# Optimization experiments

Hardware: AMD Instinct MI355X
Metric: run time of the kernel (lower is better)

## Reference

```python
import jax, jax.numpy as jnp
import numpy as np

N_ENTITY = 64368
N_REL = 40
DIM = 128
N_BASES = 8
N_EDGES = 500000
BATCH = 64
SEED_LEN = 32


def _glorot(k, shape, gain=1.414):
    fan_in, fan_out = shape[0], shape[1]
    bound = gain * np.sqrt(6.0 / (fan_in + fan_out))
    return jax.random.uniform(k, shape, jnp.float32, -bound, bound)


def setup_inputs() -> dict:
    key = jax.random.key(0)
    ks = jax.random.split(key, 11)
    return dict(
        seed_ids=jax.random.randint(ks[0], (BATCH, SEED_LEN), 0, N_ENTITY),
        edge_src=jax.random.randint(ks[1], (N_EDGES,), 0, N_ENTITY),
        edge_dst=jax.random.randint(ks[2], (N_EDGES,), 0, N_ENTITY),
        edge_type=jax.random.randint(ks[3], (N_EDGES,), 0, N_REL),
        basis=jax.random.normal(ks[4], (N_BASES, N_ENTITY, DIM), jnp.float32) * 0.02,
        att=jax.random.normal(ks[5], (N_REL, N_BASES), jnp.float32) * 0.1,
        root=jax.random.normal(ks[6], (N_ENTITY, DIM), jnp.float32) * 0.02,
        rgcn_bias=jnp.zeros((DIM,), jnp.float32),
        attn_a=_glorot(ks[7], (DIM, DIM)),
        attn_b=_glorot(ks[8], (DIM, 1)),
        out_bias=jnp.zeros((N_ENTITY,), jnp.float32),
    )


def _rgcn_nodes(basis, att, root, rgcn_bias, edge_src, edge_dst, edge_type):
    # RGCNConv with x=None: message for edge e is row src[e] of w[type[e]],
    # where w = att @ basis (basis decomposition); 'mean' aggregation to dst;
    # update: aggr + root + bias.
    n_entity, dim = root.shape
    coeff = att[edge_type]  # [E, nb]
    agg = jnp.zeros((n_entity, dim), jnp.float32)
    for b in range(basis.shape[0]):  # small fixed loop over bases
        m = basis[b][edge_src] * coeff[:, b][:, None]  # [E, dim]
        agg = agg + jax.ops.segment_sum(m, edge_dst, num_segments=n_entity)
    deg = jax.ops.segment_sum(jnp.ones_like(edge_dst, jnp.float32), edge_dst,
                              num_segments=n_entity)
    agg = agg / jnp.maximum(deg, 1.0)[:, None]
    return agg + root + rgcn_bias[None, :]


def reference(seed_ids, edge_src, edge_dst, edge_type, basis, att, root,
              rgcn_bias, attn_a, attn_b, out_bias):
    nodes = _rgcn_nodes(basis, att, root, rgcn_bias, edge_src, edge_dst, edge_type)
    # self-attention pooling over each seed set (all entries valid / non-empty)
    H = nodes[seed_ids]  # [B, S, D]
    e = jnp.einsum('bsd,d->bs', jnp.tanh(jnp.einsum('bsd,de->bse', H, attn_a)),
                   attn_b[:, 0])  # [B, S]
    attn = jax.nn.softmax(e, axis=-1)
    u = jnp.einsum('bs,bsd->bd', attn, H)  # [B, D]
    # scores = F.linear(u, nodes_features, output.bias)
    scores = u @ nodes.T + out_bias[None, :]  # [B, n_entity]
    return scores
```

## Files before the change

kernel.cpp:

```cpp
#include <hip/hip_runtime.h>
#include <hip/hip_bf16.h>

#define N_ENTITY 64368
#define N_REL 40
#define DIM 128
#define N_BASES 8
#define N_EDGES 500000
#define BATCH 64
#define SEED_LEN 32
#define NROWS (BATCH * SEED_LEN)
#define SCAN_NB ((N_ENTITY + 255) / 256)
#define NPAD (SCAN_NB * 256)

__global__ __launch_bounds__(256) void k_hist2(
    const int* __restrict__ edst, const int* __restrict__ esrc,
    int* __restrict__ hist2)
{
    int e = blockIdx.x * 256 + threadIdx.x;
    if (e < N_EDGES) {
        atomicAdd(&hist2[edst[e]], 1);
        atomicAdd(&hist2[NPAD + esrc[e]], 1);
    }
}

__global__ __launch_bounds__(256) void k_scan1(
    const int* __restrict__ hist2, int* __restrict__ ptr2,
    int* __restrict__ partial)
{
    __shared__ int s[256];
    int tid = threadIdx.x;
    int gid = blockIdx.x * 256 + tid;
    int v = hist2[gid];
    s[tid] = v;
    __syncthreads();
    for (int off = 1; off < 256; off <<= 1) {
        int t = (tid >= off) ? s[tid - off] : 0;
        __syncthreads();
        s[tid] += t;
        __syncthreads();
    }
    ptr2[gid] = s[tid] - v;
    if (tid == 255) partial[blockIdx.x] = s[255];
}

__global__ __launch_bounds__(256) void k_scan2(
    const int* __restrict__ partial, int* __restrict__ poff)
{
    __shared__ int s[256];
    int tid = threadIdx.x;
    int base = blockIdx.x * SCAN_NB;
    int v = (tid < SCAN_NB) ? partial[base + tid] : 0;
    s[tid] = v;
    __syncthreads();
    for (int off = 1; off < 256; off <<= 1) {
        int t = (tid >= off) ? s[tid - off] : 0;
        __syncthreads();
        s[tid] += t;
        __syncthreads();
    }
    if (tid < SCAN_NB) poff[base + tid] = s[tid] - v;
}

__global__ __launch_bounds__(256) void k_scan3(
    int* __restrict__ ptr2, const int* __restrict__ poff,
    int* __restrict__ work2)
{
    int gid = blockIdx.x * 256 + threadIdx.x;
    int p = ptr2[gid] + poff[blockIdx.x];
    ptr2[gid] = p;
    work2[gid] = p;
}

__global__ __launch_bounds__(256) void k_scatter2(
    const int* __restrict__ esrc, const int* __restrict__ edst,
    const int* __restrict__ etype, int* __restrict__ work2,
    int* __restrict__ payload)
{
    int e = blockIdx.x * 256 + threadIdx.x;
    if (e < N_EDGES) {
        int dpos = atomicAdd(&work2[edst[e]], 1);
        int spos = atomicAdd(&work2[NPAD + esrc[e]], 1);
        payload[spos] = dpos * 64 + etype[e];
    }
}

__global__ __launch_bounds__(256) void k_scatterD(
    const int* __restrict__ esrc, const int* __restrict__ edst,
    const int* __restrict__ etype, int* __restrict__ work2,
    int* __restrict__ meta)
{
    int e = blockIdx.x * 256 + threadIdx.x;
    if (e < N_EDGES) {
        int pos = atomicAdd(&work2[edst[e]], 1);
        meta[pos] = esrc[e] * 64 + etype[e];
    }
}

__global__ __launch_bounds__(256) void k_phaseA(
    const int* __restrict__ sptr, const int* __restrict__ shist,
    const int* __restrict__ payload, const float* __restrict__ basis,
    const float* __restrict__ att, float* __restrict__ msg)
{
    __shared__ float att_s[N_REL * N_BASES];
    int tid = threadIdx.x;
    for (int i = tid; i < N_REL * N_BASES; i += 256) att_s[i] = att[i];
    __syncthreads();

    int sid = (blockIdx.x * 256 + tid) >> 5;
    int l32 = tid & 31;
    if (sid >= N_ENTITY) return;
    int cnt = shist[sid];
    if (cnt == 0) return;
    int p = sptr[sid];

    const size_t bstride = (size_t)N_ENTITY * DIM;
    const float* bp = basis + (size_t)sid * DIM + l32 * 4;
    float4 r0 = *(const float4*)(bp + 0 * bstride);
    float4 r1 = *(const float4*)(bp + 1 * bstride);
    float4 r2 = *(const float4*)(bp + 2 * bstride);
    float4 r3 = *(const float4*)(bp + 3 * bstride);
    float4 r4 = *(const float4*)(bp + 4 * bstride);
    float4 r5 = *(const float4*)(bp + 5 * bstride);
    float4 r6 = *(const float4*)(bp + 6 * bstride);
    float4 r7 = *(const float4*)(bp + 7 * bstride);

    int j = 0;
    for (; j + 1 < cnt; j += 2) {
        int plA = payload[p + j];
        int plB = payload[p + j + 1];
        const float* cA = att_s + (plA & 63) * N_BASES;
        const float* cB = att_s + (plB & 63) * N_BASES;
        float4 cA0 = *(const float4*)(cA);
        float4 cA1 = *(const float4*)(cA + 4);
        float4 cB0 = *(const float4*)(cB);
        float4 cB1 = *(const float4*)(cB + 4);

        float4 mA, mB;
        mA.x = cA0.x*r0.x + cA0.y*r1.x + cA0.z*r2.x + cA0.w*r3.x
             + cA1.x*r4.x + cA1.y*r5.x + cA1.z*r6.x + cA1.w*r7.x;
        mA.y = cA0.x*r0.y + cA0.y*r1.y + cA0.z*r2.y + cA0.w*r3.y
             + cA1.x*r4.y + cA1.y*r5.y + cA1.z*r6.y + cA1.w*r7.y;
        mA.z = cA0.x*r0.z + cA0.y*r1.z + cA0.z*r2.z + cA0.w*r3.z
             + cA1.x*r4.z + cA1.y*r5.z + cA1.z*r6.z + cA1.w*r7.z;
        mA.w = cA0.x*r0.w + cA0.y*r1.w + cA0.z*r2.w + cA0.w*r3.w
             + cA1.x*r4.w + cA1.y*r5.w + cA1.z*r6.w + cA1.w*r7.w;
        mB.x = cB0.x*r0.x + cB0.y*r1.x + cB0.z*r2.x + cB0.w*r3.x
             + cB1.x*r4.x + cB1.y*r5.x + cB1.z*r6.x + cB1.w*r7.x;
        mB.y = cB0.x*r0.y + cB0.y*r1.y + cB0.z*r2.y + cB0.w*r3.y
             + cB1.x*r4.y + cB1.y*r5.y + cB1.z*r6.y + cB1.w*r7.y;
        mB.z = cB0.x*r0.z + cB0.y*r1.z + cB0.z*r2.z + cB0.w*r3.z
             + cB1.x*r4.z + cB1.y*r5.z + cB1.z*r6.z + cB1.w*r7.z;
        mB.w = cB0.x*r0.w + cB0.y*r1.w + cB0.z*r2.w + cB0.w*r3.w
             + cB1.x*r4.w + cB1.y*r5.w + cB1.z*r6.w + cB1.w*r7.w;

        *(float4*)(msg + (size_t)(plA >> 6) * DIM + l32 * 4) = mA;
        *(float4*)(msg + (size_t)(plB >> 6) * DIM + l32 * 4) = mB;
    }
    if (j < cnt) {
        int plA = payload[p + j];
        const float* cA = att_s + (plA & 63) * N_BASES;
        float4 cA0 = *(const float4*)(cA);
        float4 cA1 = *(const float4*)(cA + 4);
        float4 mA;
        mA.x = cA0.x*r0.x + cA0.y*r1.x + cA0.z*r2.x + cA0.w*r3.x
             + cA1.x*r4.x + cA1.y*r5.x + cA1.z*r6.x + cA1.w*r7.x;
        mA.y = cA0.x*r0.y + cA0.y*r1.y + cA0.z*r2.y + cA0.w*r3.y
             + cA1.x*r4.y + cA1.y*r5.y + cA1.z*r6.y + cA1.w*r7.y;
        mA.z = cA0.x*r0.z + cA0.y*r1.z + cA0.z*r2.z + cA0.w*r3.z
             + cA1.x*r4.z + cA1.y*r5.z + cA1.z*r6.z + cA1.w*r7.z;
        mA.w = cA0.x*r0.w + cA0.y*r1.w + cA0.z*r2.w + cA0.w*r3.w
             + cA1.x*r4.w + cA1.y*r5.w + cA1.z*r6.w + cA1.w*r7.w;
        *(float4*)(msg + (size_t)(plA >> 6) * DIM + l32 * 4) = mA;
    }
}

__global__ __launch_bounds__(256) void k_phaseB(
    const int* __restrict__ dptr, const int* __restrict__ dhist,
    const float* __restrict__ msg, const float* __restrict__ root,
    const float* __restrict__ bias, float* __restrict__ agg)
{
    int wid  = (int)((blockIdx.x * 256 + threadIdx.x) >> 6);
    int lane = threadIdx.x & 63;
    if (wid >= N_ENTITY) return;
    int cnt = dhist[wid];
    int p   = dptr[wid];
    const float* mp = msg + (size_t)p * DIM + lane * 2;

    float ax = 0.f, ay = 0.f;
    int j = 0;
    for (; j + 3 < cnt; j += 4) {
        float2 v0 = *(const float2*)(mp + (size_t)(j + 0) * DIM);
        float2 v1 = *(const float2*)(mp + (size_t)(j + 1) * DIM);
        float2 v2 = *(const float2*)(mp + (size_t)(j + 2) * DIM);
        float2 v3 = *(const float2*)(mp + (size_t)(j + 3) * DIM);
        ax += (v0.x + v1.x) + (v2.x + v3.x);
        ay += (v0.y + v1.y) + (v2.y + v3.y);
    }
    for (; j < cnt; ++j) {
        float2 v = *(const float2*)(mp + (size_t)j * DIM);
        ax += v.x; ay += v.y;
    }

    float inv = 1.0f / fmaxf((float)cnt, 1.0f);
    int o = wid * DIM + lane * 2;
    float2 r  = *(const float2*)(root + o);
    float2 bb = *(const float2*)(bias + lane * 2);
    float2 outv;
    outv.x = ax * inv + r.x + bb.x;
    outv.y = ay * inv + r.y + bb.y;
    *(float2*)(agg + o) = outv;
}

#define ACC8(C0, C1, V0, V1, V2, V3, V4, V5, V6, V7)                         \
    acc.x += C0.x*V0.x + C0.y*V1.x + C0.z*V2.x + C0.w*V3.x                   \
           + C1.x*V4.x + C1.y*V5.x + C1.z*V6.x + C1.w*V7.x;                  \
    acc.y += C0.x*V0.y + C0.y*V1.y + C0.z*V2.y + C0.w*V3.y                   \
           + C1.x*V4.y + C1.y*V5.y + C1.z*V6.y + C1.w*V7.y;                  \
    acc.z += C0.x*V0.z + C0.y*V1.z + C0.z*V2.z + C0.w*V3.z                   \
           + C1.x*V4.z + C1.y*V5.z + C1.z*V6.z + C1.w*V7.z;                  \
    acc.w += C0.x*V0.w + C0.y*V1.w + C0.z*V2.w + C0.w*V3.w                   \
           + C1.x*V4.w + C1.y*V5.w + C1.z*V6.w + C1.w*V7.w;

__global__ __launch_bounds__(256) void k_gather(
    const int* __restrict__ ptr, const int* __restrict__ hist,
    const int* __restrict__ meta, const float* __restrict__ basis,
    const float* __restrict__ att, const float* __restrict__ root,
    const float* __restrict__ bias, float* __restrict__ agg)
{
    __shared__ float att_s[N_REL * N_BASES];
    int tid = threadIdx.x;
    for (int i = tid; i < N_REL * N_BASES; i += 256) att_s[i] = att[i];
    __syncthreads();

    int wid  = (int)((blockIdx.x * 256 + tid) >> 6);
    int lane = tid & 63;
    if (wid >= N_ENTITY) return;

    int half = lane >> 5;
    int l32  = lane & 31;
    int p   = ptr[wid];
    int cnt = hist[wid];
    const size_t bstride = (size_t)N_ENTITY * DIM;

    float4 acc = {0.f, 0.f, 0.f, 0.f};
    int j = 0;
    for (; j + 3 < cnt; j += 4) {
        int mA0 = meta[p + j + 0];
        int mA1 = meta[p + j + 1];
        int mB0 = meta[p + j + 2];
        int mB1 = meta[p + j + 3];
        int mA = half ? mA1 : mA0;
        int mB = half ? mB1 : mB0;
        const float* bA = basis + (size_t)(mA >> 6) * DIM + l32 * 4;
        const float* bB = basis + (size_t)(mB >> 6) * DIM + l32 * 4;
        float4 a0 = *(const float4*)(bA + 0 * bstride);
        float4 a1 = *(const float4*)(bA + 1 * bstride);
        float4 a2 = *(const float4*)(bA + 2 * bstride);
        float4 a3 = *(const float4*)(bA + 3 * bstride);
        float4 a4 = *(const float4*)(bA + 4 * bstride);
        float4 a5 = *(const float4*)(bA + 5 * bstride);
        float4 a6 = *(const float4*)(bA + 6 * bstride);
        float4 a7 = *(const float4*)(bA + 7 * bstride);
        float4 b0 = *(const float4*)(bB + 0 * bstride);
        float4 b1 = *(const float4*)(bB + 1 * bstride);
        float4 b2 = *(const float4*)(bB + 2 * bstride);
        float4 b3 = *(const float4*)(bB + 3 * bstride);
        float4 b4 = *(const float4*)(bB + 4 * bstride);
        float4 b5 = *(const float4*)(bB + 5 * bstride);
        float4 b6 = *(const float4*)(bB + 6 * bstride);
        float4 b7 = *(const float4*)(bB + 7 * bstride);
        float4 cA0 = *(const float4*)(att_s + (mA & 63) * N_BASES);
        float4 cA1 = *(const float4*)(att_s + (mA & 63) * N_BASES + 4);
        float4 cB0 = *(const float4*)(att_s + (mB & 63) * N_BASES);
        float4 cB1 = *(const float4*)(att_s + (mB & 63) * N_BASES + 4);
        ACC8(cA0, cA1, a0, a1, a2, a3, a4, a5, a6, a7)
        ACC8(cB0, cB1, b0, b1, b2, b3, b4, b5, b6, b7)
    }
    for (; j < cnt; j += 2) {
        int m0 = meta[p + j];
        bool has1 = (j + 1 < cnt);
        int m1 = has1 ? meta[p + j + 1] : m0;
        int m = half ? m1 : m0;
        float sc = (half && !has1) ? 0.0f : 1.0f;
        const float* bA = basis + (size_t)(m >> 6) * DIM + l32 * 4;
        float4 a0 = *(const float4*)(bA + 0 * bstride);
        float4 a1 = *(const float4*)(bA + 1 * bstride);
        float4 a2 = *(const float4*)(bA + 2 * bstride);
        float4 a3 = *(const float4*)(bA + 3 * bstride);
        float4 a4 = *(const float4*)(bA + 4 * bstride);
        float4 a5 = *(const float4*)(bA + 5 * bstride);
        float4 a6 = *(const float4*)(bA + 6 * bstride);
        float4 a7 = *(const float4*)(bA + 7 * bstride);
        float4 c0 = *(const float4*)(att_s + (m & 63) * N_BASES);
        float4 c1 = *(const float4*)(att_s + (m & 63) * N_BASES + 4);
        c0.x *= sc; c0.y *= sc; c0.z *= sc; c0.w *= sc;
        c1.x *= sc; c1.y *= sc; c1.z *= sc; c1.w *= sc;
        ACC8(c0, c1, a0, a1, a2, a3, a4, a5, a6, a7)
    }

    acc.x += __shfl_xor(acc.x, 32, 64);
    acc.y += __shfl_xor(acc.y, 32, 64);
    acc.z += __shfl_xor(acc.z, 32, 64);
    acc.w += __shfl_xor(acc.w, 32, 64);

    if (half == 0) {
        float inv = 1.0f / fmaxf((float)cnt, 1.0f);
        int o = wid * DIM + l32 * 4;
        float4 r  = *(const float4*)(root + o);
        float4 bb = *(const float4*)(bias + l32 * 4);
        float4 outv;
        outv.x = acc.x * inv + r.x + bb.x;
        outv.y = acc.y * inv + r.y + bb.y;
        outv.z = acc.z * inv + r.z + bb.z;
        outv.w = acc.w * inv + r.w + bb.w;
        *(float4*)(agg + o) = outv;
    }
}

__global__ __launch_bounds__(256) void k_attn_gemm(
    const int* __restrict__ seed_ids, const float* __restrict__ nodes,
    const float* __restrict__ A, float* __restrict__ T)
{
    __shared__ float As[DIM * 132];
    __shared__ float Hs[16 * DIM];

    int tid = threadIdx.x;
    int r0  = blockIdx.x * 16;

    for (int i = tid; i < DIM * DIM; i += 256) {
        int row = i >> 7, col = i & 127;
        As[row * 132 + col] = A[i];
    }
    for (int i = tid; i < 16 * DIM; i += 256) {
        int rr = i >> 7, d = i & 127;
        int nid = seed_ids[r0 + rr];
        Hs[rr * DIM + d] = nodes[(size_t)nid * DIM + d];
    }
    __syncthreads();

    int jx = tid & 31;
    int iy = tid >> 5;
    float acc[2][4] = {{0,0,0,0},{0,0,0,0}};

    for (int d = 0; d < DIM; ++d) {
        float h0 = Hs[(iy * 2 + 0) * DIM + d];
        float h1 = Hs[(iy * 2 + 1) * DIM + d];
        const float4 a4 = *(const float4*)(As + d * 132 + jx * 4);
        acc[0][0] += h0 * a4.x; acc[0][1] += h0 * a4.y;
        acc[0][2] += h0 * a4.z; acc[0][3] += h0 * a4.w;
        acc[1][0] += h1 * a4.x; acc[1][1] += h1 * a4.y;
        acc[1][2] += h1 * a4.z; acc[1][3] += h1 * a4.w;
    }
    #pragma unroll
    for (int i = 0; i < 2; ++i) {
        int r = r0 + iy * 2 + i;
        #pragma unroll
        for (int k = 0; k < 4; ++k)
            T[(size_t)r * DIM + jx * 4 + k] = tanhf(acc[i][k]);
    }
}

__global__ __launch_bounds__(256) void k_attn_pool(
    const int* __restrict__ seed_ids, const float* __restrict__ nodes,
    const float* __restrict__ T, const float* __restrict__ Bv,
    float* __restrict__ u, float* __restrict__ uT)
{
    __shared__ float part[SEED_LEN][9];
    __shared__ float attw[SEED_LEN];

    int b = blockIdx.x, tid = threadIdx.x;
    int s = tid >> 3, g = tid & 7;

    float pe = 0.0f;
    for (int jj = g; jj < DIM; jj += 8)
        pe += T[(size_t)(b * SEED_LEN + s) * DIM + jj] * Bv[jj];
    part[s][g] = pe;
    __syncthreads();

    if (tid < SEED_LEN) {
        float e = 0.0f;
        for (int k = 0; k < 8; ++k) e += part[tid][k];
        attw[tid] = e;
    }
    __syncthreads();

    if (tid == 0) {
        float mx = -1e30f;
        for (int k = 0; k < SEED_LEN; ++k) mx = fmaxf(mx, attw[k]);
        float ssum = 0.0f;
        for (int k = 0; k < SEED_LEN; ++k) {
            float v = expf(attw[k] - mx);
            attw[k] = v; ssum += v;
        }
        float inv = 1.0f / ssum;
        for (int k = 0; k < SEED_LEN; ++k) attw[k] *= inv;
    }
    __syncthreads();

    if (tid < DIM) {
        float acc = 0.0f;
        for (int k = 0; k < SEED_LEN; ++k) {
            int nid = seed_ids[b * SEED_LEN + k];
            acc += attw[k] * nodes[(size_t)nid * DIM + tid];
        }
        u[b * DIM + tid]  = acc;
        uT[tid * BATCH + b] = acc;
    }
}

__global__ __launch_bounds__(256) void k_scores(
    const float* __restrict__ nodes, const float* __restrict__ uT,
    const float* __restrict__ out_bias, float* __restrict__ out)
{
    __shared__ float Nl[DIM * 65];

    int tid = threadIdx.x;
    int n0  = blockIdx.x * 64;

    for (int i = tid; i < 64 * DIM; i += 256) {
        int n = i >> 7, d = i & 127;
        int gn = n0 + n;
        Nl[d * 65 + n] = (gn < N_ENTITY) ? nodes[(size_t)gn * DIM + d] : 0.0f;
    }
    __syncthreads();

    int w    = __builtin_amdgcn_readfirstlane(tid >> 6);
    int lane = tid & 63;
    int b0   = w * 16;

    float acc[16];
    #pragma unroll
    for (int k = 0; k < 16; ++k) acc[k] = 0.0f;

    #pragma unroll 4
    for (int d = 0; d < DIM; ++d) {
        float nv = Nl[d * 65 + lane];
        const float* up = uT + d * BATCH + b0;
        #pragma unroll
        for (int k = 0; k < 16; ++k) acc[k] += up[k] * nv;
    }

    int gn = n0 + lane;
    if (gn < N_ENTITY) {
        float ob = out_bias[gn];
        #pragma unroll
        for (int k = 0; k < 16; ++k)
            out[(size_t)(b0 + k) * N_ENTITY + gn] = acc[k] + ob;
    }
}

extern "C" void kernel_launch(void* const* d_in, const int* in_sizes, int n_in,
                              void* d_out, int out_size, void* d_ws, size_t ws_size,
                              hipStream_t stream)
{
    const int*   seed_ids  = (const int*)d_in[0];
    const int*   esrc      = (const int*)d_in[1];
    const int*   edst      = (const int*)d_in[2];
    const int*   etype     = (const int*)d_in[3];
    const float* basis     = (const float*)d_in[4];
    const float* att       = (const float*)d_in[5];
    const float* root      = (const float*)d_in[6];
    const float* rgcn_bias = (const float*)d_in[7];
    const float* attn_a    = (const float*)d_in[8];
    const float* attn_b    = (const float*)d_in[9];
    const float* out_bias  = (const float*)d_in[10];
    float* out = (float*)d_out;

    const size_t AGG_F  = (size_t)N_ENTITY * DIM;
    const size_t MSG_F  = (size_t)N_EDGES * DIM;
    const size_t H2_I   = (size_t)2 * NPAD;

    const size_t main_words = AGG_F + MSG_F + 3 * H2_I + 1024
                            + N_EDGES + (size_t)NROWS * DIM + 2 * BATCH * DIM;
    bool big = ws_size >= main_words * 4;

    if (big) {
        float* agg     = (float*)d_ws;
        float* msg     = agg + AGG_F;
        int*   hist2   = (int*)(msg + MSG_F);
        int*   ptr2    = hist2 + H2_I;
        int*   work2   = ptr2 + H2_I;
        int*   part2   = work2 + H2_I;
        int*   poff2   = part2 + 512;
        int*   payload = poff2 + 512;
        float* T       = (float*)(payload + N_EDGES);
        float* u       = T + (size_t)NROWS * DIM;
        float* uT      = u + BATCH * DIM;

        hipMemsetAsync(hist2, 0, H2_I * sizeof(int), stream);
        k_hist2<<<(N_EDGES + 255) / 256, 256, 0, stream>>>(edst, esrc, hist2);
        k_scan1<<<2 * SCAN_NB, 256, 0, stream>>>(hist2, ptr2, part2);
        k_scan2<<<2, 256, 0, stream>>>(part2, poff2);
        k_scan3<<<2 * SCAN_NB, 256, 0, stream>>>(ptr2, poff2, work2);
        k_scatter2<<<(N_EDGES + 255) / 256, 256, 0, stream>>>(
            esrc, edst, etype, work2, payload);

        k_phaseA<<<N_ENTITY / 8, 256, 0, stream>>>(
            ptr2 + NPAD, hist2 + NPAD, payload, basis, att, msg);
        k_phaseB<<<N_ENTITY / 4, 256, 0, stream>>>(
            ptr2, hist2, msg, root, rgcn_bias, agg);

        k_attn_gemm<<<NROWS / 16, 256, 0, stream>>>(seed_ids, agg, attn_a, T);
        k_attn_pool<<<BATCH, 256, 0, stream>>>(seed_ids, agg, T, attn_b, u, uT);
        k_scores<<<(N_ENTITY + 63) / 64, 256, 0, stream>>>(agg, uT, out_bias, out);
    } else {
        float* agg     = (float*)d_ws;
        int*   hist2   = (int*)(agg + AGG_F);
        int*   ptr2    = hist2 + H2_I;
        int*   work2   = ptr2 + H2_I;
        int*   part2   = work2 + H2_I;
        int*   poff2   = part2 + 512;
        int*   meta    = poff2 + 512;
        float* T       = (float*)(meta + N_EDGES);
        float* u       = T + (size_t)NROWS * DIM;
        float* uT      = u + BATCH * DIM;

        hipMemsetAsync(hist2, 0, H2_I * sizeof(int), stream);
        k_hist2<<<(N_EDGES + 255) / 256, 256, 0, stream>>>(edst, esrc, hist2);
        k_scan1<<<2 * SCAN_NB, 256, 0, stream>>>(hist2, ptr2, part2);
        k_scan2<<<2, 256, 0, stream>>>(part2, poff2);
        k_scan3<<<2 * SCAN_NB, 256, 0, stream>>>(ptr2, poff2, work2);
        k_scatterD<<<(N_EDGES + 255) / 256, 256, 0, stream>>>(
            esrc, edst, etype, work2, meta);

        k_gather<<<(N_ENTITY * 64 + 255) / 256, 256, 0, stream>>>(
            ptr2, hist2, meta, basis, att, root, rgcn_bias, agg);

        k_attn_gemm<<<NROWS / 16, 256, 0, stream>>>(seed_ids, agg, attn_a, T);
        k_attn_pool<<<BATCH, 256, 0, stream>>>(seed_ids, agg, T, attn_b, u, uT);
        k_scores<<<(N_ENTITY + 63) / 64, 256, 0, stream>>>(agg, uT, out_bias, out);
    }
}
```

Before: 626.3 us.

## Replace message buffer with float atomics into aggregate, sort edges by source only

Phase A now adds each per-edge message straight into the node aggregate with unsafe float atomics, instead of writing a 256MB per-edge message buffer that Phase B then reduced by destination. Only the source-side CSR is built, which removes one atomic per edge in the scatter and the dual-size workspace branch. A light finalize kernel applies the mean, root and bias. In exchange there is heavy atomic traffic on random destination rows and a non-deterministic float summation order.

```diff
diff --git a/kernel.cpp b/kernel.cpp
--- a/kernel.cpp
+++ b/kernel.cpp
@@ -24,13 +24,13 @@
 }
 
 __global__ __launch_bounds__(256) void k_scan1(
-    const int* __restrict__ hist2, int* __restrict__ ptr2,
+    const int* __restrict__ shist, int* __restrict__ sptr,
     int* __restrict__ partial)
 {
     __shared__ int s[256];
     int tid = threadIdx.x;
     int gid = blockIdx.x * 256 + tid;
-    int v = hist2[gid];
+    int v = shist[gid];
     s[tid] = v;
     __syncthreads();
     for (int off = 1; off < 256; off <<= 1) {
@@ -39,7 +39,7 @@
         s[tid] += t;
         __syncthreads();
     }
-    ptr2[gid] = s[tid] - v;
+    sptr[gid] = s[tid] - v;
     if (tid == 255) partial[blockIdx.x] = s[255];
 }
 
@@ -48,8 +48,7 @@
 {
     __shared__ int s[256];
     int tid = threadIdx.x;
-    int base = blockIdx.x * SCAN_NB;
-    int v = (tid < SCAN_NB) ? partial[base + tid] : 0;
+    int v = (tid < SCAN_NB) ? partial[tid] : 0;
     s[tid] = v;
     __syncthreads();
     for (int off = 1; off < 256; off <<= 1) {
@@ -58,48 +57,35 @@
         s[tid] += t;
         __syncthreads();
     }
-    if (tid < SCAN_NB) poff[base + tid] = s[tid] - v;
+    if (tid < SCAN_NB) poff[tid] = s[tid] - v;
 }
 
 __global__ __launch_bounds__(256) void k_scan3(
-    int* __restrict__ ptr2, const int* __restrict__ poff,
-    int* __restrict__ work2)
+    int* __restrict__ sptr, const int* __restrict__ poff,
+    int* __restrict__ swork)
 {
     int gid = blockIdx.x * 256 + threadIdx.x;
-    int p = ptr2[gid] + poff[blockIdx.x];
-    ptr2[gid] = p;
-    work2[gid] = p;
-}
-
-__global__ __launch_bounds__(256) void k_scatter2(
+    int p = sptr[gid] + poff[blockIdx.x];
+    sptr[gid] = p;
+    swork[gid] = p;
+}
+
+__global__ __launch_bounds__(256) void k_scatterS(
     const int* __restrict__ esrc, const int* __restrict__ edst,
-    const int* __restrict__ etype, int* __restrict__ work2,
+    const int* __restrict__ etype, int* __restrict__ swork,
     int* __restrict__ payload)
 {
     int e = blockIdx.x * 256 + threadIdx.x;
     if (e < N_EDGES) {
-        int dpos = atomicAdd(&work2[edst[e]], 1);
-        int spos = atomicAdd(&work2[NPAD + esrc[e]], 1);
-        payload[spos] = dpos * 64 + etype[e];
-    }
-}
-
-__global__ __launch_bounds__(256) void k_scatterD(
-    const int* __restrict__ esrc, const int* __restrict__ edst,
-    const int* __restrict__ etype, int* __restrict__ work2,
-    int* __restrict__ meta)
-{
-    int e = blockIdx.x * 256 + threadIdx.x;
-    if (e < N_EDGES) {
-        int pos = atomicAdd(&work2[edst[e]], 1);
-        meta[pos] = esrc[e] * 64 + etype[e];
-    }
-}
-
-__global__ __launch_bounds__(256) void k_phaseA(
+        int spos = atomicAdd(&swork[esrc[e]], 1);
+        payload[spos] = edst[e] * 64 + etype[e];
+    }
+}
+
+__global__ __launch_bounds__(256) void k_phaseA_atomic(
     const int* __restrict__ sptr, const int* __restrict__ shist,
     const int* __restrict__ payload, const float* __restrict__ basis,
-    const float* __restrict__ att, float* __restrict__ msg)
+    const float* __restrict__ att, float* __restrict__ agg)
 {
     __shared__ float att_s[N_REL * N_BASES];
     int tid = threadIdx.x;
@@ -153,8 +139,16 @@
         mB.w = cB0.x*r0.w + cB0.y*r1.w + cB0.z*r2.w + cB0.w*r3.w
              + cB1.x*r4.w + cB1.y*r5.w + cB1.z*r6.w + cB1.w*r7.w;
 
-        *(float4*)(msg + (size_t)(plA >> 6) * DIM + l32 * 4) = mA;
-        *(float4*)(msg + (size_t)(plB >> 6) * DIM + l32 * 4) = mB;
+        float* dA = agg + (size_t)(plA >> 6) * DIM + l32 * 4;
+        float* dB = agg + (size_t)(plB >> 6) * DIM + l32 * 4;
+        unsafeAtomicAdd(dA + 0, mA.x);
+        unsafeAtomicAdd(dA + 1, mA.y);
+        unsafeAtomicAdd(dA + 2, mA.z);
+        unsafeAtomicAdd(dA + 3, mA.w);
+        unsafeAtomicAdd(dB + 0, mB.x);
+        unsafeAtomicAdd(dB + 1, mB.y);
+        unsafeAtomicAdd(dB + 2, mB.z);
+        unsafeAtomicAdd(dB + 3, mB.w);
     }
     if (j < cnt) {
         int plA = payload[p + j];
@@ -170,151 +164,32 @@
              + cA1.x*r4.z + cA1.y*r5.z + cA1.z*r6.z + cA1.w*r7.z;
         mA.w = cA0.x*r0.w + cA0.y*r1.w + cA0.z*r2.w + cA0.w*r3.w
              + cA1.x*r4.w + cA1.y*r5.w + cA1.z*r6.w + cA1.w*r7.w;
-        *(float4*)(msg + (size_t)(plA >> 6) * DIM + l32 * 4) = mA;
-    }
-}
-
-__global__ __launch_bounds__(256) void k_phaseB(
-    const int* __restrict__ dptr, const int* __restrict__ dhist,
-    const float* __restrict__ msg, const float* __restrict__ root,
+        float* dA = agg + (size_t)(plA >> 6) * DIM + l32 * 4;
+        unsafeAtomicAdd(dA + 0, mA.x);
+        unsafeAtomicAdd(dA + 1, mA.y);
+        unsafeAtomicAdd(dA + 2, mA.z);
+        unsafeAtomicAdd(dA + 3, mA.w);
+    }
+}
+
+__global__ __launch_bounds__(256) void k_finalize(
+    const int* __restrict__ dhist, const float* __restrict__ root,
     const float* __restrict__ bias, float* __restrict__ agg)
 {
-    int wid  = (int)((blockIdx.x * 256 + threadIdx.x) >> 6);
-    int lane = threadIdx.x & 63;
+    int gid = blockIdx.x * 256 + threadIdx.x;
+    int wid = gid >> 5;
+    int l32 = gid & 31;
     if (wid >= N_ENTITY) return;
-    int cnt = dhist[wid];
-    int p   = dptr[wid];
-    const float* mp = msg + (size_t)p * DIM + lane * 2;
-
-    float ax = 0.f, ay = 0.f;
-    int j = 0;
-    for (; j + 3 < cnt; j += 4) {
-        float2 v0 = *(const float2*)(mp + (size_t)(j + 0) * DIM);
-        float2 v1 = *(const float2*)(mp + (size_t)(j + 1) * DIM);
-        float2 v2 = *(const float2*)(mp + (size_t)(j + 2) * DIM);
-        float2 v3 = *(const float2*)(mp + (size_t)(j + 3) * DIM);
-        ax += (v0.x + v1.x) + (v2.x + v3.x);
-        ay += (v0.y + v1.y) + (v2.y + v3.y);
-    }
-    for (; j < cnt; ++j) {
-        float2 v = *(const float2*)(mp + (size_t)j * DIM);
-        ax += v.x; ay += v.y;
-    }
-
-    float inv = 1.0f / fmaxf((float)cnt, 1.0f);
-    int o = wid * DIM + lane * 2;
-    float2 r  = *(const float2*)(root + o);
-    float2 bb = *(const float2*)(bias + lane * 2);
-    float2 outv;
-    outv.x = ax * inv + r.x + bb.x;
-    outv.y = ay * inv + r.y + bb.y;
-    *(float2*)(agg + o) = outv;
-}
-
-#define ACC8(C0, C1, V0, V1, V2, V3, V4, V5, V6, V7)                         \
-    acc.x += C0.x*V0.x + C0.y*V1.x + C0.z*V2.x + C0.w*V3.x                   \
-           + C1.x*V4.x + C1.y*V5.x + C1.z*V6.x + C1.w*V7.x;                  \
-    acc.y += C0.x*V0.y + C0.y*V1.y + C0.z*V2.y + C0.w*V3.y                   \
-           + C1.x*V4.y + C1.y*V5.y + C1.z*V6.y + C1.w*V7.y;                  \
-    acc.z += C0.x*V0.z + C0.y*V1.z + C0.z*V2.z + C0.w*V3.z                   \
-           + C1.x*V4.z + C1.y*V5.z + C1.z*V6.z + C1.w*V7.z;                  \
-    acc.w += C0.x*V0.w + C0.y*V1.w + C0.z*V2.w + C0.w*V3.w                   \
-           + C1.x*V4.w + C1.y*V5.w + C1.z*V6.w + C1.w*V7.w;
-
-__global__ __launch_bounds__(256) void k_gather(
-    const int* __restrict__ ptr, const int* __restrict__ hist,
-    const int* __restrict__ meta, const float* __restrict__ basis,
-    const float* __restrict__ att, const float* __restrict__ root,
-    const float* __restrict__ bias, float* __restrict__ agg)
-{
-    __shared__ float att_s[N_REL * N_BASES];
-    int tid = threadIdx.x;
-    for (int i = tid; i < N_REL * N_BASES; i += 256) att_s[i] = att[i];
-    __syncthreads();
-
-    int wid  = (int)((blockIdx.x * 256 + tid) >> 6);
-    int lane = tid & 63;
-    if (wid >= N_ENTITY) return;
-
-    int half = lane >> 5;
-    int l32  = lane & 31;
-    int p   = ptr[wid];
-    int cnt = hist[wid];
-    const size_t bstride = (size_t)N_ENTITY * DIM;
-
-    float4 acc = {0.f, 0.f, 0.f, 0.f};
-    int j = 0;
-    for (; j + 3 < cnt; j += 4) {
-        int mA0 = meta[p + j + 0];
-        int mA1 = meta[p + j + 1];
-        int mB0 = meta[p + j + 2];
-        int mB1 = meta[p + j + 3];
-        int mA = half ? mA1 : mA0;
-        int mB = half ? mB1 : mB0;
-        const float* bA = basis + (size_t)(mA >> 6) * DIM + l32 * 4;
-        const float* bB = basis + (size_t)(mB >> 6) * DIM + l32 * 4;
-        float4 a0 = *(const float4*)(bA + 0 * bstride);
-        float4 a1 = *(const float4*)(bA + 1 * bstride);
-        float4 a2 = *(const float4*)(bA + 2 * bstride);
-        float4 a3 = *(const float4*)(bA + 3 * bstride);
-        float4 a4 = *(const float4*)(bA + 4 * bstride);
-        float4 a5 = *(const float4*)(bA + 5 * bstride);
-        float4 a6 = *(const float4*)(bA + 6 * bstride);
-        float4 a7 = *(const float4*)(bA + 7 * bstride);
-        float4 b0 = *(const float4*)(bB + 0 * bstride);
-        float4 b1 = *(const float4*)(bB + 1 * bstride);
-        float4 b2 = *(const float4*)(bB + 2 * bstride);
-        float4 b3 = *(const float4*)(bB + 3 * bstride);
-        float4 b4 = *(const float4*)(bB + 4 * bstride);
-        float4 b5 = *(const float4*)(bB + 5 * bstride);
-        float4 b6 = *(const float4*)(bB + 6 * bstride);
-        float4 b7 = *(const float4*)(bB + 7 * bstride);
-        float4 cA0 = *(const float4*)(att_s + (mA & 63) * N_BASES);
-        float4 cA1 = *(const float4*)(att_s + (mA & 63) * N_BASES + 4);
-        float4 cB0 = *(const float4*)(att_s + (mB & 63) * N_BASES);
-        float4 cB1 = *(const float4*)(att_s + (mB & 63) * N_BASES + 4);
-        ACC8(cA0, cA1, a0, a1, a2, a3, a4, a5, a6, a7)
-        ACC8(cB0, cB1, b0, b1, b2, b3, b4, b5, b6, b7)
-    }
-    for (; j < cnt; j += 2) {
-        int m0 = meta[p + j];
-        bool has1 = (j + 1 < cnt);
-        int m1 = has1 ? meta[p + j + 1] : m0;
-        int m = half ? m1 : m0;
-        float sc = (half && !has1) ? 0.0f : 1.0f;
-        const float* bA = basis + (size_t)(m >> 6) * DIM + l32 * 4;
-        float4 a0 = *(const float4*)(bA + 0 * bstride);
-        float4 a1 = *(const float4*)(bA + 1 * bstride);
-        float4 a2 = *(const float4*)(bA + 2 * bstride);
-        float4 a3 = *(const float4*)(bA + 3 * bstride);
-        float4 a4 = *(const float4*)(bA + 4 * bstride);
-        float4 a5 = *(const float4*)(bA + 5 * bstride);
-        float4 a6 = *(const float4*)(bA + 6 * bstride);
-        float4 a7 = *(const float4*)(bA + 7 * bstride);
-        float4 c0 = *(const float4*)(att_s + (m & 63) * N_BASES);
-        float4 c1 = *(const float4*)(att_s + (m & 63) * N_BASES + 4);
-        c0.x *= sc; c0.y *= sc; c0.z *= sc; c0.w *= sc;
-        c1.x *= sc; c1.y *= sc; c1.z *= sc; c1.w *= sc;
-        ACC8(c0, c1, a0, a1, a2, a3, a4, a5, a6, a7)
-    }
-
-    acc.x += __shfl_xor(acc.x, 32, 64);
-    acc.y += __shfl_xor(acc.y, 32, 64);
-    acc.z += __shfl_xor(acc.z, 32, 64);
-    acc.w += __shfl_xor(acc.w, 32, 64);
-
-    if (half == 0) {
-        float inv = 1.0f / fmaxf((float)cnt, 1.0f);
-        int o = wid * DIM + l32 * 4;
-        float4 r  = *(const float4*)(root + o);
-        float4 bb = *(const float4*)(bias + l32 * 4);
-        float4 outv;
-        outv.x = acc.x * inv + r.x + bb.x;
-        outv.y = acc.y * inv + r.y + bb.y;
-        outv.z = acc.z * inv + r.z + bb.z;
-        outv.w = acc.w * inv + r.w + bb.w;
-        *(float4*)(agg + o) = outv;
-    }
+    float inv = 1.0f / fmaxf((float)dhist[wid], 1.0f);
+    int o = wid * DIM + l32 * 4;
+    float4 a  = *(const float4*)(agg + o);
+    float4 r  = *(const float4*)(root + o);
+    float4 bb = *(const float4*)(bias + l32 * 4);
+    a.x = a.x * inv + r.x + bb.x;
+    a.y = a.y * inv + r.y + bb.y;
+    a.z = a.z * inv + r.z + bb.z;
+    a.w = a.w * inv + r.w + bb.w;
+    *(float4*)(agg + o) = a;
 }
 
 __global__ __launch_bounds__(256) void k_attn_gemm(
@@ -466,68 +341,34 @@
     const float* out_bias  = (const float*)d_in[10];
     float* out = (float*)d_out;
 
-    const size_t AGG_F  = (size_t)N_ENTITY * DIM;
-    const size_t MSG_F  = (size_t)N_EDGES * DIM;
-    const size_t H2_I   = (size_t)2 * NPAD;
-
-    const size_t main_words = AGG_F + MSG_F + 3 * H2_I + 1024
-                            + N_EDGES + (size_t)NROWS * DIM + 2 * BATCH * DIM;
-    bool big = ws_size >= main_words * 4;
-
-    if (big) {
-        float* agg     = (float*)d_ws;
-        float* msg     = agg + AGG_F;
-        int*   hist2   = (int*)(msg + MSG_F);
-        int*   ptr2    = hist2 + H2_I;
-        int*   work2   = ptr2 + H2_I;
-        int*   part2   = work2 + H2_I;
-        int*   poff2   = part2 + 512;
-        int*   payload = poff2 + 512;
-        float* T       = (float*)(payload + N_EDGES);
-        float* u       = T + (size_t)NROWS * DIM;
-        float* uT      = u + BATCH * DIM;
-
-        hipMemsetAsync(hist2, 0, H2_I * sizeof(int), stream);
-        k_hist2<<<(N_EDGES + 255) / 256, 256, 0, stream>>>(edst, esrc, hist2);
-        k_scan1<<<2 * SCAN_NB, 256, 0, stream>>>(hist2, ptr2, part2);
-        k_scan2<<<2, 256, 0, stream>>>(part2, poff2);
-        k_scan3<<<2 * SCAN_NB, 256, 0, stream>>>(ptr2, poff2, work2);
-        k_scatter2<<<(N_EDGES + 255) / 256, 256, 0, stream>>>(
-            esrc, edst, etype, work2, payload);
-
-        k_phaseA<<<N_ENTITY / 8, 256, 0, stream>>>(
-            ptr2 + NPAD, hist2 + NPAD, payload, basis, att, msg);
-        k_phaseB<<<N_ENTITY / 4, 256, 0, stream>>>(
-            ptr2, hist2, msg, root, rgcn_bias, agg);
-
-        k_attn_gemm<<<NROWS / 16, 256, 0, stream>>>(seed_ids, agg, attn_a, T);
-        k_attn_pool<<<BATCH, 256, 0, stream>>>(seed_ids, agg, T, attn_b, u, uT);
-        k_scores<<<(N_ENTITY + 63) / 64, 256, 0, stream>>>(agg, uT, out_bias, out);
-    } else {
-        float* agg     = (float*)d_ws;
-        int*   hist2   = (int*)(agg + AGG_F);
-        int*   ptr2    = hist2 + H2_I;
-        int*   work2   = ptr2 + H2_I;
-        int*   part2   = work2 + H2_I;
-        int*   poff2   = part2 + 512;
-        int*   meta    = poff2 + 512;
-        float* T       = (float*)(meta + N_EDGES);
-        float* u       = T + (size_t)NROWS * DIM;
-        float* uT      = u + BATCH * DIM;
-
-        hipMemsetAsync(hist2, 0, H2_I * sizeof(int), stream);
-        k_hist2<<<(N_EDGES + 255) / 256, 256, 0, stream>>>(edst, esrc, hist2);
-        k_scan1<<<2 * SCAN_NB, 256, 0, stream>>>(hist2, ptr2, part2);
-        k_scan2<<<2, 256, 0, stream>>>(part2, poff2);
-        k_scan3<<<2 * SCAN_NB, 256, 0, stream>>>(ptr2, poff2, work2);
-        k_scatterD<<<(N_EDGES + 255) / 256, 256, 0, stream>>>(
-            esrc, edst, etype, work2, meta);
-
-        k_gather<<<(N_ENTITY * 64 + 255) / 256, 256, 0, stream>>>(
-            ptr2, hist2, meta, basis, att, root, rgcn_bias, agg);
-
-        k_attn_gemm<<<NROWS / 16, 256, 0, stream>>>(seed_ids, agg, attn_a, T);
-        k_attn_pool<<<BATCH, 256, 0, stream>>>(seed_ids, agg, T, attn_b, u, uT);
-        k_scores<<<(N_ENTITY + 63) / 64, 256, 0, stream>>>(agg, uT, out_bias, out);
-    }
-}
+    const size_t AGG_F = (size_t)N_ENTITY * DIM;
+
+    float* agg     = (float*)d_ws;
+    int*   hist2   = (int*)(agg + AGG_F);
+    int*   sptr    = hist2 + 2 * NPAD;
+    int*   swork   = sptr + NPAD;
+    int*   part    = swork + NPAD;
+    int*   poff    = part + 256;
+    int*   payload = poff + 256;
+    float* T       = (float*)(payload + N_EDGES);
+    float* u       = T + (size_t)NROWS * DIM;
+    float* uT      = u + BATCH * DIM;
+
+    hipMemsetAsync(d_ws, 0, (AGG_F + 2 * NPAD) * sizeof(float), stream);
+
+    k_hist2<<<(N_EDGES + 255) / 256, 256, 0, stream>>>(edst, esrc, hist2);
+    k_scan1<<<SCAN_NB, 256, 0, stream>>>(hist2 + NPAD, sptr, part);
+    k_scan2<<<1, 256, 0, stream>>>(part, poff);
+    k_scan3<<<SCAN_NB, 256, 0, stream>>>(sptr, poff, swork);
+    k_scatterS<<<(N_EDGES + 255) / 256, 256, 0, stream>>>(
+        esrc, edst, etype, swork, payload);
+
+    k_phaseA_atomic<<<N_ENTITY / 8, 256, 0, stream>>>(
+        sptr, hist2 + NPAD, payload, basis, att, agg);
+    k_finalize<<<(N_ENTITY * 32 + 255) / 256, 256, 0, stream>>>(
+        hist2, root, rgcn_bias, agg);
+
+    k_attn_gemm<<<NROWS / 16, 256, 0, stream>>>(seed_ids, agg, attn_a, T);
+    k_attn_pool<<<BATCH, 256, 0, stream>>>(seed_ids, agg, T, attn_b, u, uT);
+    k_scores<<<(N_ENTITY + 63) / 64, 256, 0, stream>>>(agg, uT, out_bias, out);
+}
```

Result: slower. 1.276 ms (+103.7%).

## Store edge messages in fp16 in source order and gather them via index

Applied to the files above, without the earlier changes.

Phase A now writes each edge message contiguously in source-sorted order, stored as half precision instead of fp32. Scatter writes a per-destination index array pointing at the source-sorted slot. Phase B then gathers half2 messages through that index rather than reading a destination-contiguous fp32 buffer. This halves the intermediate message traffic and makes the phase A writes sequential, in exchange for scattered reads in phase B and fp16 rounding of each message.

```diff
diff --git a/kernel.cpp b/kernel.cpp
--- a/kernel.cpp
+++ b/kernel.cpp
@@ -1,5 +1,6 @@
 #include <hip/hip_runtime.h>
 #include <hip/hip_bf16.h>
+#include <hip/hip_fp16.h>
 
 #define N_ENTITY 64368
 #define N_REL 40
@@ -12,6 +13,8 @@
 #define SCAN_NB ((N_ENTITY + 255) / 256)
 #define NPAD (SCAN_NB * 256)
 
+struct alignas(8) half4 { __half2 lo, hi; };
+
 __global__ __launch_bounds__(256) void k_hist2(
     const int* __restrict__ edst, const int* __restrict__ esrc,
     int* __restrict__ hist2)
@@ -74,13 +77,14 @@
 __global__ __launch_bounds__(256) void k_scatter2(
     const int* __restrict__ esrc, const int* __restrict__ edst,
     const int* __restrict__ etype, int* __restrict__ work2,
-    int* __restrict__ payload)
+    int* __restrict__ ptype, int* __restrict__ idx)
 {
     int e = blockIdx.x * 256 + threadIdx.x;
     if (e < N_EDGES) {
+        int spos = atomicAdd(&work2[NPAD + esrc[e]], 1);
         int dpos = atomicAdd(&work2[edst[e]], 1);
-        int spos = atomicAdd(&work2[NPAD + esrc[e]], 1);
-        payload[spos] = dpos * 64 + etype[e];
+        ptype[spos] = etype[e];
+        idx[dpos] = spos;
     }
 }
 
@@ -98,8 +102,8 @@
 
 __global__ __launch_bounds__(256) void k_phaseA(
     const int* __restrict__ sptr, const int* __restrict__ shist,
-    const int* __restrict__ payload, const float* __restrict__ basis,
-    const float* __restrict__ att, float* __restrict__ msg)
+    const int* __restrict__ ptype, const float* __restrict__ basis,
+    const float* __restrict__ att, __half* __restrict__ msg)
 {
     __shared__ float att_s[N_REL * N_BASES];
     int tid = threadIdx.x;
@@ -126,10 +130,10 @@
 
     int j = 0;
     for (; j + 1 < cnt; j += 2) {
-        int plA = payload[p + j];
-        int plB = payload[p + j + 1];
-        const float* cA = att_s + (plA & 63) * N_BASES;
-        const float* cB = att_s + (plB & 63) * N_BASES;
+        int tA = ptype[p + j];
+        int tB = ptype[p + j + 1];
+        const float* cA = att_s + tA * N_BASES;
+        const float* cB = att_s + tB * N_BASES;
         float4 cA0 = *(const float4*)(cA);
         float4 cA1 = *(const float4*)(cA + 4);
         float4 cB0 = *(const float4*)(cB);
@@ -153,12 +157,17 @@
         mB.w = cB0.x*r0.w + cB0.y*r1.w + cB0.z*r2.w + cB0.w*r3.w
              + cB1.x*r4.w + cB1.y*r5.w + cB1.z*r6.w + cB1.w*r7.w;
 
-        *(float4*)(msg + (size_t)(plA >> 6) * DIM + l32 * 4) = mA;
-        *(float4*)(msg + (size_t)(plB >> 6) * DIM + l32 * 4) = mB;
+        half4 hA, hB;
+        hA.lo = __floats2half2_rn(mA.x, mA.y);
+        hA.hi = __floats2half2_rn(mA.z, mA.w);
+        hB.lo = __floats2half2_rn(mB.x, mB.y);
+        hB.hi = __floats2half2_rn(mB.z, mB.w);
+        *(half4*)(msg + ((size_t)(p + j)     << 7) + (l32 << 2)) = hA;
+        *(half4*)(msg + ((size_t)(p + j + 1) << 7) + (l32 << 2)) = hB;
     }
     if (j < cnt) {
-        int plA = payload[p + j];
-        const float* cA = att_s + (plA & 63) * N_BASES;
+        int tA = ptype[p + j];
+        const float* cA = att_s + tA * N_BASES;
         float4 cA0 = *(const float4*)(cA);
         float4 cA1 = *(const float4*)(cA + 4);
         float4 mA;
@@ -170,35 +179,48 @@
              + cA1.x*r4.z + cA1.y*r5.z + cA1.z*r6.z + cA1.w*r7.z;
         mA.w = cA0.x*r0.w + cA0.y*r1.w + cA0.z*r2.w + cA0.w*r3.w
              + cA1.x*r4.w + cA1.y*r5.w + cA1.z*r6.w + cA1.w*r7.w;
-        *(float4*)(msg + (size_t)(plA >> 6) * DIM + l32 * 4) = mA;
+        half4 hA;
+        hA.lo = __floats2half2_rn(mA.x, mA.y);
+        hA.hi = __floats2half2_rn(mA.z, mA.w);
+        *(half4*)(msg + ((size_t)(p + j) << 7) + (l32 << 2)) = hA;
     }
 }
 
 __global__ __launch_bounds__(256) void k_phaseB(
     const int* __restrict__ dptr, const int* __restrict__ dhist,
-    const float* __restrict__ msg, const float* __restrict__ root,
-    const float* __restrict__ bias, float* __restrict__ agg)
+    const int* __restrict__ idx, const __half* __restrict__ msg,
+    const float* __restrict__ root, const float* __restrict__ bias,
+    float* __restrict__ agg)
 {
     int wid  = (int)((blockIdx.x * 256 + threadIdx.x) >> 6);
     int lane = threadIdx.x & 63;
     if (wid >= N_ENTITY) return;
     int cnt = dhist[wid];
     int p   = dptr[wid];
-    const float* mp = msg + (size_t)p * DIM + lane * 2;
+    const __half2* mp = (const __half2*)msg;
 
     float ax = 0.f, ay = 0.f;
     int j = 0;
     for (; j + 3 < cnt; j += 4) {
-        float2 v0 = *(const float2*)(mp + (size_t)(j + 0) * DIM);
-        float2 v1 = *(const float2*)(mp + (size_t)(j + 1) * DIM);
-        float2 v2 = *(const float2*)(mp + (size_t)(j + 2) * DIM);
-        float2 v3 = *(const float2*)(mp + (size_t)(j + 3) * DIM);
-        ax += (v0.x + v1.x) + (v2.x + v3.x);
-        ay += (v0.y + v1.y) + (v2.y + v3.y);
+        int i0 = idx[p + j + 0];
+        int i1 = idx[p + j + 1];
+        int i2 = idx[p + j + 2];
+        int i3 = idx[p + j + 3];
+        __half2 v0 = mp[((size_t)i0 << 6) + lane];
+        __half2 v1 = mp[((size_t)i1 << 6) + lane];
+        __half2 v2 = mp[((size_t)i2 << 6) + lane];
+        __half2 v3 = mp[((size_t)i3 << 6) + lane];
+        float2 f0 = __half22float2(v0);
+        float2 f1 = __half22float2(v1);
+        float2 f2 = __half22float2(v2);
+        float2 f3 = __half22float2(v3);
+        ax += (f0.x + f1.x) + (f2.x + f3.x);
+        ay += (f0.y + f1.y) + (f2.y + f3.y);
     }
     for (; j < cnt; ++j) {
-        float2 v = *(const float2*)(mp + (size_t)j * DIM);
-        ax += v.x; ay += v.y;
+        int i0 = idx[p + j];
+        float2 f = __half22float2(mp[((size_t)i0 << 6) + lane]);
+        ax += f.x; ay += f.y;
     }
 
     float inv = 1.0f / fmaxf((float)cnt, 1.0f);
@@ -467,25 +489,27 @@
     float* out = (float*)d_out;
 
     const size_t AGG_F  = (size_t)N_ENTITY * DIM;
-    const size_t MSG_F  = (size_t)N_EDGES * DIM;
+    const size_t MSG_W  = (size_t)N_EDGES * 64;
     const size_t H2_I   = (size_t)2 * NPAD;
 
-    const size_t main_words = AGG_F + MSG_F + 3 * H2_I + 1024
-                            + N_EDGES + (size_t)NROWS * DIM + 2 * BATCH * DIM;
+    const size_t main_words = AGG_F + MSG_W + 3 * H2_I + 1024
+                            + 2 * (size_t)N_EDGES + (size_t)NROWS * DIM
+                            + 2 * BATCH * DIM;
     bool big = ws_size >= main_words * 4;
 
     if (big) {
-        float* agg     = (float*)d_ws;
-        float* msg     = agg + AGG_F;
-        int*   hist2   = (int*)(msg + MSG_F);
-        int*   ptr2    = hist2 + H2_I;
-        int*   work2   = ptr2 + H2_I;
-        int*   part2   = work2 + H2_I;
-        int*   poff2   = part2 + 512;
-        int*   payload = poff2 + 512;
-        float* T       = (float*)(payload + N_EDGES);
-        float* u       = T + (size_t)NROWS * DIM;
-        float* uT      = u + BATCH * DIM;
+        float*  agg    = (float*)d_ws;
+        __half* msg    = (__half*)(agg + AGG_F);
+        int*    hist2  = (int*)(agg + AGG_F + MSG_W);
+        int*    ptr2   = hist2 + H2_I;
+        int*    work2  = ptr2 + H2_I;
+        int*    part2  = work2 + H2_I;
+        int*    poff2  = part2 + 512;
+        int*    ptype  = poff2 + 512;
+        int*    idx    = ptype + N_EDGES;
+        float*  T      = (float*)(idx + N_EDGES);
+        float*  u      = T + (size_t)NROWS * DIM;
+        float*  uT     = u + BATCH * DIM;
 
         hipMemsetAsync(hist2, 0, H2_I * sizeof(int), stream);
         k_hist2<<<(N_EDGES + 255) / 256, 256, 0, stream>>>(edst, esrc, hist2);
@@ -493,12 +517,12 @@
         k_scan2<<<2, 256, 0, stream>>>(part2, poff2);
         k_scan3<<<2 * SCAN_NB, 256, 0, stream>>>(ptr2, poff2, work2);
         k_scatter2<<<(N_EDGES + 255) / 256, 256, 0, stream>>>(
-            esrc, edst, etype, work2, payload);
+            esrc, edst, etype, work2, ptype, idx);
 
         k_phaseA<<<N_ENTITY / 8, 256, 0, stream>>>(
-            ptr2 + NPAD, hist2 + NPAD, payload, basis, att, msg);
+            ptr2 + NPAD, hist2 + NPAD, ptype, basis, att, msg);
         k_phaseB<<<N_ENTITY / 4, 256, 0, stream>>>(
-            ptr2, hist2, msg, root, rgcn_bias, agg);
+            ptr2, hist2, idx, msg, root, rgcn_bias, agg);
 
         k_attn_gemm<<<NROWS / 16, 256, 0, stream>>>(seed_ids, agg, attn_a, T);
         k_attn_pool<<<BATCH, 256, 0, stream>>>(seed_ids, agg, T, attn_b, u, uT);
```

Result: faster. 612.2 us (-2.3%).
